# Kernel optimization log

Measured on AMD Instinct MI355X. Metric: run time of the kernel, lower is better.

## Reference

```python
import jax, jax.numpy as jnp
import numpy as np

N_NODES = 100000
N_EDGES = 1600000
N_GRAPHS = 64
D_IN = 128
D_HID = 128
PERM = 128
N_CLS = 8


def _sage_conv(h, src, dst, W_self, W_neigh, b, n_nodes):
    # DGL SAGEConv 'mean': fc_self(h) + fc_neigh(mean of in-neighbor feats) + bias
    agg = jax.ops.segment_sum(h[src], dst, num_segments=n_nodes)          # [N, d]
    deg = jax.ops.segment_sum(jnp.ones((src.shape[0],), h.dtype), dst,
                              num_segments=n_nodes)                        # [N]
    mean = agg / jnp.maximum(deg, 1.0)[:, None]                            # zero-deg nodes -> 0
    return h @ W_self + mean @ W_neigh + b


def setup_inputs() -> dict:
    key = jax.random.key(0)
    ks = jax.random.split(key, 12)
    s = 1.0 / np.sqrt(D_IN)
    inp = {
        'h': jax.random.normal(ks[0], (N_NODES, D_IN), jnp.float32),
        'perm_features': jax.random.normal(ks[1], (N_GRAPHS, PERM), jnp.float32),
        'src': jax.random.randint(ks[2], (N_EDGES,), 0, N_NODES),
        'dst': jax.random.randint(ks[3], (N_EDGES,), 0, N_NODES),
        'graph_ids': jnp.sort(jax.random.randint(ks[4], (N_NODES,), 0, N_GRAPHS)),
        'W1_self': jax.random.normal(ks[5], (D_IN, D_HID), jnp.float32) * s,
        'W1_neigh': jax.random.normal(ks[6], (D_IN, D_HID), jnp.float32) * s,
        'b1': jnp.zeros((D_HID,), jnp.float32),
        'W2_self': jax.random.normal(ks[7], (D_HID, D_HID), jnp.float32) * s,
        'W2_neigh': jax.random.normal(ks[8], (D_HID, D_HID), jnp.float32) * s,
        'b2': jnp.zeros((D_HID,), jnp.float32),
        'Wc': jax.random.normal(ks[9], (D_HID + PERM, N_CLS), jnp.float32) * s,
        'bc': jnp.zeros((N_CLS,), jnp.float32),
    }
    return inp


def reference(h, perm_features, src, dst, graph_ids,
              W1_self, W1_neigh, b1, W2_self, W2_neigh, b2, Wc, bc):
    n = h.shape[0]
    h1 = jax.nn.relu(_sage_conv(h, src, dst, W1_self, W1_neigh, b1, n))
    h2 = _sage_conv(h1, src, dst, W2_self, W2_neigh, b2, n)
    # dgl.mean_nodes: per-graph mean of node features
    gsum = jax.ops.segment_sum(h2, graph_ids, num_segments=N_GRAPHS)       # [B, d]
    gcnt = jax.ops.segment_sum(jnp.ones((n,), h.dtype), graph_ids,
                               num_segments=N_GRAPHS)                       # [B]
    hg = gsum / jnp.maximum(gcnt, 1.0)[:, None]
    combined = jnp.concatenate([hg, perm_features], axis=1)                 # [B, d+perm]
    return combined @ Wc + bc
```

## Files before the change

kernel.cpp:

```cpp
#include <hip/hip_runtime.h>

#define DID 128
#define NCLS 8
#define NPB 512
#define NPB_SHIFT 9
#define NBLK 256
#define CAP 12288
#define PCHUNK 64

typedef __attribute__((ext_vector_type(8))) short bf16x8;
typedef __attribute__((ext_vector_type(4))) float f32x4;
typedef __attribute__((ext_vector_type(8))) unsigned short u16x8;

static __device__ __forceinline__ unsigned short f2bf(float f) {
  union { float f; unsigned int u; } x;
  x.f = f;
  unsigned int r = (x.u + 0x7fffu + ((x.u >> 16) & 1u)) >> 16;
  return (unsigned short)r;
}
static __device__ __forceinline__ float bfhi(unsigned int v) {
  union { unsigned int u; float f; } x;
  x.u = v & 0xffff0000u;
  return x.f;
}
static __device__ __forceinline__ float bflo(unsigned int v) {
  union { unsigned int u; float f; } x;
  x.u = v << 16;
  return x.f;
}
static __device__ __forceinline__ int lowerb(const int* __restrict__ a, int n,
                                             int key) {
  int lo = 0, hi = n;
  while (lo < hi) {
    int m = (lo + hi) >> 1;
    if (a[m] < key) lo = m + 1;
    else hi = m;
  }
  return lo;
}

__global__ __launch_bounds__(256) void k_prep(
    const float* __restrict__ h, unsigned short* __restrict__ hb, int total8,
    int ncvt, const float* __restrict__ W0, const float* __restrict__ W1,
    const float* __restrict__ W2, const float* __restrict__ W3,
    unsigned short* __restrict__ P0, unsigned short* __restrict__ P1,
    unsigned short* __restrict__ P2, unsigned short* __restrict__ P3,
    const int* __restrict__ dst, int* __restrict__ hist, int E, int nbuk,
    float* __restrict__ gsum, int ngsum) {
  __shared__ int c[256];
  int bid = blockIdx.x;
  int tid = threadIdx.x;
  if (bid < ncvt) {
    int i = bid * 256 + tid;
    if (i >= total8) return;
    const float4* h4 = (const float4*)h;
    float4 a = h4[(size_t)i * 2];
    float4 b = h4[(size_t)i * 2 + 1];
    u16x8 o;
    o[0] = f2bf(a.x); o[1] = f2bf(a.y); o[2] = f2bf(a.z); o[3] = f2bf(a.w);
    o[4] = f2bf(b.x); o[5] = f2bf(b.y); o[6] = f2bf(b.z); o[7] = f2bf(b.w);
    *(u16x8*)(hb + (size_t)i * 8) = o;
  } else if (bid < ncvt + 256) {
    int gid = (bid - ncvt) * 256 + tid;
    int m = gid >> 14;
    int idx = gid & 16383;
    int j = idx & 7;
    int l = (idx >> 3) & 63;
    int kf = (idx >> 9) & 3;
    int ct = idx >> 11;
    int colc = ct * 16 + (l & 15);
    int k = kf * 32 + (l >> 4) * 8 + j;
    const float* W = (m == 0) ? W0 : (m == 1) ? W1 : (m == 2) ? W2 : W3;
    unsigned short* P = (m == 0) ? P0 : (m == 1) ? P1 : (m == 2) ? P2 : P3;
    P[idx] = f2bf(W[k * 128 + colc]);
  } else if (bid < ncvt + 256 + NBLK) {
    int b = bid - ncvt - 256;
    for (int i = tid; i < nbuk; i += 256) c[i] = 0;
    __syncthreads();
    int epb = (E + NBLK - 1) / NBLK;
    int e0 = b * epb;
    int e1 = min(E, e0 + epb);
    for (int e = e0 + tid; e < e1; e += 256)
      atomicAdd(&c[dst[e] >> NPB_SHIFT], 1);
    __syncthreads();
    for (int i = tid; i < nbuk; i += 256)
      hist[(size_t)i * NBLK + b] = c[i];
  } else {
    for (int i = tid; i < ngsum; i += 256) gsum[i] = 0.f;
  }
}

__global__ void k_scan1(const int* __restrict__ deg, int* __restrict__ rp,
                        int* __restrict__ part, int n) {
  __shared__ int sd[256];
  int t = threadIdx.x;
  int base = blockIdx.x * 1024 + t * 4;
  int v0 = (base + 0 < n) ? deg[base + 0] : 0;
  int v1 = (base + 1 < n) ? deg[base + 1] : 0;
  int v2 = (base + 2 < n) ? deg[base + 2] : 0;
  int v3 = (base + 3 < n) ? deg[base + 3] : 0;
  int ts = v0 + v1 + v2 + v3;
  sd[t] = ts;
  __syncthreads();
  for (int off = 1; off < 256; off <<= 1) {
    int x = 0;
    if (t >= off) x = sd[t - off];
    __syncthreads();
    if (t >= off) sd[t] += x;
    __syncthreads();
  }
  int excl = sd[t] - ts;
  if (base + 0 < n) rp[base + 0] = excl;
  if (base + 1 < n) rp[base + 1] = excl + v0;
  if (base + 2 < n) rp[base + 2] = excl + v0 + v1;
  if (base + 3 < n) rp[base + 3] = excl + v0 + v1 + v2;
  if (t == 255) part[blockIdx.x] = sd[255];
}

__global__ void k_scan2(int* __restrict__ part, int nblk) {
  __shared__ int sd[1024];
  int t = threadIdx.x;
  int v = (t < nblk) ? part[t] : 0;
  sd[t] = v;
  __syncthreads();
  for (int off = 1; off < 1024; off <<= 1) {
    int x = 0;
    if (t >= off) x = sd[t - off];
    __syncthreads();
    if (t >= off) sd[t] += x;
    __syncthreads();
  }
  if (t < nblk) part[t] = sd[t] - v;
}

__global__ void k_scan3(int* __restrict__ rp, const int* __restrict__ part,
                        int n, int E) {
  int t = threadIdx.x;
  int add = part[blockIdx.x];
  int base = blockIdx.x * 1024 + t * 4;
#pragma unroll
  for (int i = 0; i < 4; ++i)
    if (base + i < n) rp[base + i] += add;
  if (blockIdx.x == 0 && t == 0) rp[n] = E;
}

__global__ __launch_bounds__(256) void kB_scat(const int* __restrict__ src,
                                               const int* __restrict__ dst,
                                               const int* __restrict__ off,
                                               unsigned int* __restrict__ pairs,
                                               int E, int nbuk) {
  __shared__ int cur[256];
  int tid = threadIdx.x;
  for (int i = tid; i < nbuk; i += 256)
    cur[i] = off[(size_t)i * NBLK + blockIdx.x];
  __syncthreads();
  int epb = (E + NBLK - 1) / NBLK;
  int e0 = blockIdx.x * epb;
  int e1 = min(E, e0 + epb);
  for (int e = e0 + tid; e < e1; e += 256) {
    int s = src[e];
    int d = dst[e];
    int p = atomicAdd(&cur[d >> NPB_SHIFT], 1);
    pairs[p] = ((unsigned)(d & (NPB - 1)) << 23) | (unsigned)s;
  }
}

__global__ __launch_bounds__(512) void kB_build(
    const unsigned int* __restrict__ pairs, const int* __restrict__ off,
    int* __restrict__ rp, int* __restrict__ col, int N, int nbuk, int E) {
  __shared__ int cnt[NPB];
  __shared__ int exc[NPB];
  __shared__ int colstage[CAP];
  int tid = threadIdx.x;
  int b = blockIdx.x;
  int eb = off[(size_t)b * NBLK];
  int ee = off[(size_t)(b + 1) * NBLK];
  int m = ee - eb;

  cnt[tid] = 0;
  __syncthreads();
  for (int i = eb + tid; i < ee; i += NPB) {
    int dl = (int)(pairs[i] >> 23);
    atomicAdd(&cnt[dl], 1);
  }
  __syncthreads();
  exc[tid] = cnt[tid];
  __syncthreads();
  for (int o = 1; o < NPB; o <<= 1) {
    int v = (tid >= o) ? exc[tid - o] : 0;
    __syncthreads();
    exc[tid] += v;
    __syncthreads();
  }
  int myexc = exc[tid] - cnt[tid];
  int node = b * NPB + tid;
  if (node < N) rp[node] = eb + myexc;
  if (b == nbuk - 1 && tid == 0) rp[N] = E;
  __syncthreads();
  cnt[tid] = myexc;
  __syncthreads();
  if (m <= CAP) {
    for (int i = eb + tid; i < ee; i += NPB) {
      unsigned int pr = pairs[i];
      int dl = (int)(pr >> 23);
      int s = (int)(pr & 0x7fffffu);
      int p = atomicAdd(&cnt[dl], 1);
      colstage[p] = s;
    }
    __syncthreads();
    for (int i = tid; i < m; i += NPB) col[eb + i] = colstage[i];
  } else {
    for (int i = eb + tid; i < ee; i += NPB) {
      unsigned int pr = pairs[i];
      int dl = (int)(pr >> 23);
      int s = (int)(pr & 0x7fffffu);
      int p = atomicAdd(&cnt[dl], 1);
      col[eb + p] = s;
    }
  }
}

__global__ __launch_bounds__(256, 4) void k_gemm2(
    const unsigned short* __restrict__ hb, const unsigned short* __restrict__ WpS,
    const unsigned short* __restrict__ WpN, float* __restrict__ z,
    unsigned short* __restrict__ yb, int n) {
  const int l = threadIdx.x & 63;
  const int w = threadIdx.x >> 6;
  const int rb = blockIdx.x >> 1;
  const int cb = blockIdx.x & 1;
  const int rowW = rb * 128 + w * 32;
  const int cl = l & 15;
  const int cg = l >> 4;

  bf16x8 A[2][4];
#pragma unroll
  for (int rt = 0; rt < 2; ++rt) {
    int row = rowW + rt * 16 + cl;
#pragma unroll
    for (int kf = 0; kf < 4; ++kf) {
      if (row < n)
        A[rt][kf] = *(const bf16x8*)(hb + (size_t)row * 128 + kf * 32 + cg * 8);
      else
        A[rt][kf] = (bf16x8){0, 0, 0, 0, 0, 0, 0, 0};
    }
  }

  f32x4 accS[2][4], accN[2][4];
#pragma unroll
  for (int rt = 0; rt < 2; ++rt)
#pragma unroll
    for (int ct = 0; ct < 4; ++ct) {
      accS[rt][ct] = (f32x4){0.f, 0.f, 0.f, 0.f};
      accN[rt][ct] = (f32x4){0.f, 0.f, 0.f, 0.f};
    }

#pragma unroll
  for (int ct = 0; ct < 4; ++ct) {
    int ctg = cb * 4 + ct;
    bf16x8 BS[4], BN[4];
#pragma unroll
    for (int kf = 0; kf < 4; ++kf) {
      BS[kf] = *(const bf16x8*)(WpS + ((ctg * 4 + kf) * 64 + l) * 8);
      BN[kf] = *(const bf16x8*)(WpN + ((ctg * 4 + kf) * 64 + l) * 8);
    }
#pragma unroll
    for (int rt = 0; rt < 2; ++rt)
#pragma unroll
      for (int kf = 0; kf < 4; ++kf) {
        accS[rt][ct] =
            __builtin_amdgcn_mfma_f32_16x16x32_bf16(A[rt][kf], BS[kf], accS[rt][ct], 0, 0, 0);
        accN[rt][ct] =
            __builtin_amdgcn_mfma_f32_16x16x32_bf16(A[rt][kf], BN[kf], accN[rt][ct], 0, 0, 0);
      }
  }

#pragma unroll
  for (int rt = 0; rt < 2; ++rt)
#pragma unroll
    for (int ct = 0; ct < 4; ++ct) {
      int colc = (cb * 4 + ct) * 16 + cl;
#pragma unroll
      for (int r = 0; r < 4; ++r) {
        int row = rowW + rt * 16 + cg * 4 + r;
        if (row < n) {
          z[(size_t)row * 128 + colc] = accS[rt][ct][r];
          yb[(size_t)row * 128 + colc] = f2bf(accN[rt][ct][r]);
        }
      }
    }
}

template <int OUTMODE>
__global__ __launch_bounds__(256, 8) void k_aggr2(
    const unsigned int* __restrict__ Y, const float* Z,
    const int* __restrict__ rp, const int* __restrict__ col,
    const float* __restrict__ bias, void* outp, int n) {
  int wid = (blockIdx.x * 256 + threadIdx.x) >> 6;
  int lane = threadIdx.x & 63;
  if (wid >= n) return;
  int s = rp[wid], e = rp[wid + 1];
  float ax = 0.f, ay = 0.f;
  int i = s;
  for (; i + 8 <= e; i += 8) {
    unsigned int v0 = Y[(size_t)col[i + 0] * 64 + lane];
    unsigned int v1 = Y[(size_t)col[i + 1] * 64 + lane];
    unsigned int v2 = Y[(size_t)col[i + 2] * 64 + lane];
    unsigned int v3 = Y[(size_t)col[i + 3] * 64 + lane];
    unsigned int v4 = Y[(size_t)col[i + 4] * 64 + lane];
    unsigned int v5 = Y[(size_t)col[i + 5] * 64 + lane];
    unsigned int v6 = Y[(size_t)col[i + 6] * 64 + lane];
    unsigned int v7 = Y[(size_t)col[i + 7] * 64 + lane];
    ax += bflo(v0) + bflo(v1) + bflo(v2) + bflo(v3) + bflo(v4) + bflo(v5) +
          bflo(v6) + bflo(v7);
    ay += bfhi(v0) + bfhi(v1) + bfhi(v2) + bfhi(v3) + bfhi(v4) + bfhi(v5) +
          bfhi(v6) + bfhi(v7);
  }
  for (; i + 4 <= e; i += 4) {
    unsigned int v0 = Y[(size_t)col[i + 0] * 64 + lane];
    unsigned int v1 = Y[(size_t)col[i + 1] * 64 + lane];
    unsigned int v2 = Y[(size_t)col[i + 2] * 64 + lane];
    unsigned int v3 = Y[(size_t)col[i + 3] * 64 + lane];
    ax += bflo(v0) + bflo(v1) + bflo(v2) + bflo(v3);
    ay += bfhi(v0) + bfhi(v1) + bfhi(v2) + bfhi(v3);
  }
  for (; i < e; ++i) {
    unsigned int v = Y[(size_t)col[i] * 64 + lane];
    ax += bflo(v);
    ay += bfhi(v);
  }
  int deg = e - s;
  float scale = 1.0f / (float)(deg > 1 ? deg : 1);
  float2 zv = ((const float2*)Z)[(size_t)wid * 64 + lane];
  float2 bb = ((const float2*)bias)[lane];
  float ox = zv.x + ax * scale + bb.x;
  float oy = zv.y + ay * scale + bb.y;
  if (OUTMODE == 1) {
    ox = fmaxf(ox, 0.f);
    oy = fmaxf(oy, 0.f);
    unsigned int packed = (unsigned int)f2bf(ox) | ((unsigned int)f2bf(oy) << 16);
    ((unsigned int*)outp)[(size_t)wid * 64 + lane] = packed;
  } else {
    ((float2*)outp)[(size_t)wid * 64 + lane] = make_float2(ox, oy);
  }
}

__global__ __launch_bounds__(256) void k_pool(const float* __restrict__ H2,
                                              const int* __restrict__ gids,
                                              float* __restrict__ gsum, int N) {
  int g = blockIdx.x / PCHUNK;
  int c = blockIdx.x % PCHUNK;
  int t = threadIdx.x;
  int s = lowerb(gids, N, g);
  int e = lowerb(gids, N, g + 1);
  int cnt = e - s;
  int per = (cnt + PCHUNK - 1) / PCHUNK;
  int rs = s + c * per;
  int re = rs + per < e ? rs + per : e;
  if (rs >= re) return;
  int rslot = t >> 5;
  int d4 = t & 31;
  const float4* H4 = (const float4*)H2;
  float4 acc = make_float4(0.f, 0.f, 0.f, 0.f);
  for (int r = rs + rslot; r < re; r += 8) {
    float4 v = H4[(size_t)r * 32 + d4];
    acc.x += v.x; acc.y += v.y; acc.z += v.z; acc.w += v.w;
  }
  __shared__ float4 sacc[256];
  sacc[t] = acc;
  __syncthreads();
#pragma unroll
  for (int o = 4; o >= 1; o >>= 1) {
    if (rslot < o) {
      float4 a = sacc[t];
      float4 b = sacc[t + o * 32];
      a.x += b.x; a.y += b.y; a.z += b.z; a.w += b.w;
      sacc[t] = a;
    }
    __syncthreads();
  }
  if (t < 32) {
    float4 a = sacc[t];
    atomicAdd(&gsum[g * DID + t * 4 + 0], a.x);
    atomicAdd(&gsum[g * DID + t * 4 + 1], a.y);
    atomicAdd(&gsum[g * DID + t * 4 + 2], a.z);
    atomicAdd(&gsum[g * DID + t * 4 + 3], a.w);
  }
}

__global__ void k_head(const float* __restrict__ gsum,
                       const float* __restrict__ perm,
                       const float* __restrict__ Wc,
                       const float* __restrict__ bc,
                       const int* __restrict__ gids, float* __restrict__ out,
                       int N, int NG) {
  int t = threadIdx.x;
  if (t >= NG * NCLS) return;
  int g = t >> 3, c = t & 7;
  int cnt = lowerb(gids, N, g + 1) - lowerb(gids, N, g);
  float inv = 1.0f / (float)(cnt > 1 ? cnt : 1);
  float acc = bc[c];
#pragma unroll 4
  for (int k = 0; k < DID; ++k)
    acc += gsum[g * DID + k] * inv * Wc[k * NCLS + c];
#pragma unroll 4
  for (int k = 0; k < DID; ++k)
    acc += perm[g * DID + k] * Wc[(DID + k) * NCLS + c];
  out[g * NCLS + c] = acc;
}

extern "C" void kernel_launch(void* const* d_in, const int* in_sizes, int n_in,
                              void* d_out, int out_size, void* d_ws,
                              size_t ws_size, hipStream_t stream) {
  const float* h = (const float*)d_in[0];
  const float* perm = (const float*)d_in[1];
  const int* src = (const int*)d_in[2];
  const int* dst = (const int*)d_in[3];
  const int* gids = (const int*)d_in[4];
  const float* W1s = (const float*)d_in[5];
  const float* W1n = (const float*)d_in[6];
  const float* b1 = (const float*)d_in[7];
  const float* W2s = (const float*)d_in[8];
  const float* W2n = (const float*)d_in[9];
  const float* b2 = (const float*)d_in[10];
  const float* Wc = (const float*)d_in[11];
  const float* bc = (const float*)d_in[12];
  float* out = (float*)d_out;

  const int N = in_sizes[0] / DID;
  const int E = in_sizes[2];
  const int NG = in_sizes[1] / DID;
  const int nbuk = (N + NPB - 1) >> NPB_SHIFT;
  const int nscan = nbuk * NBLK;

  char* w = (char*)d_ws;
  size_t off_ = 0;
  auto alloc = [&](size_t bytes) -> void* {
    off_ = (off_ + 511) & ~(size_t)511;
    void* p = w + off_;
    off_ += bytes;
    return p;
  };
  float* gsum = (float*)alloc((size_t)NG * DID * 4);
  int* hist = (int*)alloc((size_t)nscan * 4);
  int* boff = (int*)alloc((size_t)(nscan + 1) * 4);
  int* part = (int*)alloc(1024 * 4);
  int* rp = (int*)alloc((size_t)(N + 1) * 4);
  int* col = (int*)alloc((size_t)E * 4);
  unsigned int* pairs = (unsigned int*)alloc((size_t)E * 4);
  unsigned short* hb = (unsigned short*)alloc((size_t)N * DID * 2);
  unsigned short* yb = (unsigned short*)alloc((size_t)N * DID * 2);
  float* z = (float*)alloc((size_t)N * DID * 4);
  unsigned short* Wp1s = (unsigned short*)alloc(128 * 128 * 2);
  unsigned short* Wp1n = (unsigned short*)alloc(128 * 128 * 2);
  unsigned short* Wp2s = (unsigned short*)alloc(128 * 128 * 2);
  unsigned short* Wp2n = (unsigned short*)alloc(128 * 128 * 2);

  const int nchunk = (nscan + 1023) / 1024;
  const int ngb2 = ((N + 127) / 128) * 2;
  const int nagg = (N + 3) / 4;
  const int total8 = N * DID / 8;
  const int ncvt = (total8 + 255) / 256;

  k_prep<<<ncvt + 256 + NBLK + 1, 256, 0, stream>>>(
      h, hb, total8, ncvt, W1s, W1n, W2s, W2n, Wp1s, Wp1n, Wp2s, Wp2n, dst,
      hist, E, nbuk, gsum, NG * DID);

  k_scan1<<<nchunk, 256, 0, stream>>>(hist, boff, part, nscan);
  k_scan2<<<1, 1024, 0, stream>>>(part, nchunk);
  k_scan3<<<nchunk, 256, 0, stream>>>(boff, part, nscan, E);
  kB_scat<<<NBLK, 256, 0, stream>>>(src, dst, boff, pairs, E, nbuk);
  kB_build<<<nbuk, NPB, 0, stream>>>(pairs, boff, rp, col, N, nbuk, E);

  k_gemm2<<<ngb2, 256, 0, stream>>>(hb, Wp1s, Wp1n, z, yb, N);
  k_aggr2<1><<<nagg, 256, 0, stream>>>((const unsigned int*)yb, z, rp, col, b1,
                                       (void*)hb, N);

  k_gemm2<<<ngb2, 256, 0, stream>>>(hb, Wp2s, Wp2n, z, yb, N);
  k_aggr2<0><<<nagg, 256, 0, stream>>>((const unsigned int*)yb, z, rp, col, b2,
                                       (void*)z, N);

  k_pool<<<NG * PCHUNK, 256, 0, stream>>>(z, gids, gsum, N);
  k_head<<<1, 512, 0, stream>>>(gsum, perm, Wc, bc, gids, out, N, NG);
}
```

Before: 421.0 us.

## Merge pipeline stages into fewer launches and fuse pool with head

Cuts the launch count by merging stages. The three-kernel scan becomes a single-block scan, and the bf16 conversion of h runs alongside it. The edge scatter and the first GEMM share one launch. The GEMM now computes all 128 columns per block rather than splitting columns across two blocks. Pooling and the classifier head are fused through a global atomic counter that block 0 spin-waits on, which assumes all blocks become resident and adds a serialized single-block scan.

```diff
diff --git a/kernel.cpp b/kernel.cpp
--- a/kernel.cpp
+++ b/kernel.cpp
@@ -6,7 +6,7 @@
 #define NPB_SHIFT 9
 #define NBLK 256
 #define CAP 12288
-#define PCHUNK 64
+#define PCHUNK 16
 
 typedef __attribute__((ext_vector_type(8))) short bf16x8;
 typedef __attribute__((ext_vector_type(4))) float f32x4;
@@ -39,29 +39,28 @@
   return lo;
 }
 
-__global__ __launch_bounds__(256) void k_prep(
-    const float* __restrict__ h, unsigned short* __restrict__ hb, int total8,
-    int ncvt, const float* __restrict__ W0, const float* __restrict__ W1,
+__global__ __launch_bounds__(256) void kA_hpz(
+    const int* __restrict__ dst, int* __restrict__ hist, int E, int nbuk,
+    const float* __restrict__ W0, const float* __restrict__ W1,
     const float* __restrict__ W2, const float* __restrict__ W3,
     unsigned short* __restrict__ P0, unsigned short* __restrict__ P1,
     unsigned short* __restrict__ P2, unsigned short* __restrict__ P3,
-    const int* __restrict__ dst, int* __restrict__ hist, int E, int nbuk,
     float* __restrict__ gsum, int ngsum) {
   __shared__ int c[256];
-  int bid = blockIdx.x;
-  int tid = threadIdx.x;
-  if (bid < ncvt) {
-    int i = bid * 256 + tid;
-    if (i >= total8) return;
-    const float4* h4 = (const float4*)h;
-    float4 a = h4[(size_t)i * 2];
-    float4 b = h4[(size_t)i * 2 + 1];
-    u16x8 o;
-    o[0] = f2bf(a.x); o[1] = f2bf(a.y); o[2] = f2bf(a.z); o[3] = f2bf(a.w);
-    o[4] = f2bf(b.x); o[5] = f2bf(b.y); o[6] = f2bf(b.z); o[7] = f2bf(b.w);
-    *(u16x8*)(hb + (size_t)i * 8) = o;
-  } else if (bid < ncvt + 256) {
-    int gid = (bid - ncvt) * 256 + tid;
+  int bid = blockIdx.x, tid = threadIdx.x;
+  if (bid < NBLK) {
+    for (int i = tid; i < nbuk; i += 256) c[i] = 0;
+    __syncthreads();
+    int epb = (E + NBLK - 1) / NBLK;
+    int e0 = bid * epb;
+    int e1 = min(E, e0 + epb);
+    for (int e = e0 + tid; e < e1; e += 256)
+      atomicAdd(&c[dst[e] >> NPB_SHIFT], 1);
+    __syncthreads();
+    for (int i = tid; i < nbuk; i += 256)
+      hist[(size_t)i * NBLK + bid] = c[i];
+  } else if (bid < NBLK + 256) {
+    int gid = (bid - NBLK) * 256 + tid;
     int m = gid >> 14;
     int idx = gid & 16383;
     int j = idx & 7;
@@ -73,96 +72,149 @@
     const float* W = (m == 0) ? W0 : (m == 1) ? W1 : (m == 2) ? W2 : W3;
     unsigned short* P = (m == 0) ? P0 : (m == 1) ? P1 : (m == 2) ? P2 : P3;
     P[idx] = f2bf(W[k * 128 + colc]);
-  } else if (bid < ncvt + 256 + NBLK) {
-    int b = bid - ncvt - 256;
-    for (int i = tid; i < nbuk; i += 256) c[i] = 0;
-    __syncthreads();
-    int epb = (E + NBLK - 1) / NBLK;
-    int e0 = b * epb;
-    int e1 = min(E, e0 + epb);
-    for (int e = e0 + tid; e < e1; e += 256)
-      atomicAdd(&c[dst[e] >> NPB_SHIFT], 1);
-    __syncthreads();
-    for (int i = tid; i < nbuk; i += 256)
-      hist[(size_t)i * NBLK + b] = c[i];
   } else {
     for (int i = tid; i < ngsum; i += 256) gsum[i] = 0.f;
   }
 }
 
-__global__ void k_scan1(const int* __restrict__ deg, int* __restrict__ rp,
-                        int* __restrict__ part, int n) {
-  __shared__ int sd[256];
-  int t = threadIdx.x;
-  int base = blockIdx.x * 1024 + t * 4;
-  int v0 = (base + 0 < n) ? deg[base + 0] : 0;
-  int v1 = (base + 1 < n) ? deg[base + 1] : 0;
-  int v2 = (base + 2 < n) ? deg[base + 2] : 0;
-  int v3 = (base + 3 < n) ? deg[base + 3] : 0;
-  int ts = v0 + v1 + v2 + v3;
-  sd[t] = ts;
-  __syncthreads();
-  for (int off = 1; off < 256; off <<= 1) {
-    int x = 0;
-    if (t >= off) x = sd[t - off];
-    __syncthreads();
-    if (t >= off) sd[t] += x;
-    __syncthreads();
-  }
-  int excl = sd[t] - ts;
-  if (base + 0 < n) rp[base + 0] = excl;
-  if (base + 1 < n) rp[base + 1] = excl + v0;
-  if (base + 2 < n) rp[base + 2] = excl + v0 + v1;
-  if (base + 3 < n) rp[base + 3] = excl + v0 + v1 + v2;
-  if (t == 255) part[blockIdx.x] = sd[255];
-}
-
-__global__ void k_scan2(int* __restrict__ part, int nblk) {
-  __shared__ int sd[1024];
-  int t = threadIdx.x;
-  int v = (t < nblk) ? part[t] : 0;
-  sd[t] = v;
-  __syncthreads();
-  for (int off = 1; off < 1024; off <<= 1) {
-    int x = 0;
-    if (t >= off) x = sd[t - off];
-    __syncthreads();
-    if (t >= off) sd[t] += x;
-    __syncthreads();
-  }
-  if (t < nblk) part[t] = sd[t] - v;
-}
-
-__global__ void k_scan3(int* __restrict__ rp, const int* __restrict__ part,
-                        int n, int E) {
-  int t = threadIdx.x;
-  int add = part[blockIdx.x];
-  int base = blockIdx.x * 1024 + t * 4;
-#pragma unroll
-  for (int i = 0; i < 4; ++i)
-    if (base + i < n) rp[base + i] += add;
-  if (blockIdx.x == 0 && t == 0) rp[n] = E;
-}
-
-__global__ __launch_bounds__(256) void kB_scat(const int* __restrict__ src,
-                                               const int* __restrict__ dst,
-                                               const int* __restrict__ off,
-                                               unsigned int* __restrict__ pairs,
-                                               int E, int nbuk) {
-  __shared__ int cur[256];
+__global__ __launch_bounds__(256) void kB_scan_h2b(
+    const int* __restrict__ hist, int* __restrict__ boff, int nbuk, int E,
+    const float* __restrict__ h, unsigned short* __restrict__ hb, int total8) {
   int tid = threadIdx.x;
-  for (int i = tid; i < nbuk; i += 256)
-    cur[i] = off[(size_t)i * NBLK + blockIdx.x];
-  __syncthreads();
-  int epb = (E + NBLK - 1) / NBLK;
-  int e0 = blockIdx.x * epb;
-  int e1 = min(E, e0 + epb);
-  for (int e = e0 + tid; e < e1; e += 256) {
-    int s = src[e];
-    int d = dst[e];
-    int p = atomicAdd(&cur[d >> NPB_SHIFT], 1);
-    pairs[p] = ((unsigned)(d & (NPB - 1)) << 23) | (unsigned)s;
-  }
+  if (blockIdx.x == 0) {
+    __shared__ int sd[256];
+    int seg = nbuk;
+    int base = tid * seg;
+    int ssum = 0;
+    for (int i = 0; i < seg; ++i) ssum += hist[base + i];
+    sd[tid] = ssum;
+    __syncthreads();
+    for (int o = 1; o < 256; o <<= 1) {
+      int x = (tid >= o) ? sd[tid - o] : 0;
+      __syncthreads();
+      sd[tid] += x;
+      __syncthreads();
+    }
+    int run = sd[tid] - ssum;
+    for (int i = 0; i < seg; ++i) {
+      int v = hist[base + i];
+      boff[base + i] = run;
+      run += v;
+    }
+    if (tid == 255) boff[(size_t)nbuk * NBLK] = E;
+  } else {
+    int i = (blockIdx.x - 1) * 256 + tid;
+    if (i >= total8) return;
+    const float4* h4 = (const float4*)h;
+    float4 a = h4[(size_t)i * 2];
+    float4 b = h4[(size_t)i * 2 + 1];
+    u16x8 o;
+    o[0] = f2bf(a.x); o[1] = f2bf(a.y); o[2] = f2bf(a.z); o[3] = f2bf(a.w);
+    o[4] = f2bf(b.x); o[5] = f2bf(b.y); o[6] = f2bf(b.z); o[7] = f2bf(b.w);
+    *(u16x8*)(hb + (size_t)i * 8) = o;
+  }
+}
+
+__device__ __forceinline__ void gemm_body(
+    int bid, const unsigned short* __restrict__ hb,
+    const unsigned short* __restrict__ WpS,
+    const unsigned short* __restrict__ WpN, float* __restrict__ z,
+    unsigned short* __restrict__ yb, int n) {
+  const int l = threadIdx.x & 63;
+  const int w = threadIdx.x >> 6;
+  const int rowW = bid * 128 + w * 32;
+  const int cl = l & 15;
+  const int cg = l >> 4;
+
+  bf16x8 A[2][4];
+#pragma unroll
+  for (int rt = 0; rt < 2; ++rt) {
+    int row = rowW + rt * 16 + cl;
+#pragma unroll
+    for (int kf = 0; kf < 4; ++kf) {
+      if (row < n)
+        A[rt][kf] = *(const bf16x8*)(hb + (size_t)row * 128 + kf * 32 + cg * 8);
+      else
+        A[rt][kf] = (bf16x8){0, 0, 0, 0, 0, 0, 0, 0};
+    }
+  }
+
+  f32x4 accS[2][8], accN[2][8];
+#pragma unroll
+  for (int rt = 0; rt < 2; ++rt)
+#pragma unroll
+    for (int ct = 0; ct < 8; ++ct) {
+      accS[rt][ct] = (f32x4){0.f, 0.f, 0.f, 0.f};
+      accN[rt][ct] = (f32x4){0.f, 0.f, 0.f, 0.f};
+    }
+
+#pragma unroll
+  for (int ct = 0; ct < 8; ++ct) {
+    bf16x8 BS[4], BN[4];
+#pragma unroll
+    for (int kf = 0; kf < 4; ++kf) {
+      BS[kf] = *(const bf16x8*)(WpS + ((ct * 4 + kf) * 64 + l) * 8);
+      BN[kf] = *(const bf16x8*)(WpN + ((ct * 4 + kf) * 64 + l) * 8);
+    }
+#pragma unroll
+    for (int rt = 0; rt < 2; ++rt)
+#pragma unroll
+      for (int kf = 0; kf < 4; ++kf) {
+        accS[rt][ct] =
+            __builtin_amdgcn_mfma_f32_16x16x32_bf16(A[rt][kf], BS[kf], accS[rt][ct], 0, 0, 0);
+        accN[rt][ct] =
+            __builtin_amdgcn_mfma_f32_16x16x32_bf16(A[rt][kf], BN[kf], accN[rt][ct], 0, 0, 0);
+      }
+  }
+
+#pragma unroll
+  for (int rt = 0; rt < 2; ++rt)
+#pragma unroll
+    for (int ct = 0; ct < 8; ++ct) {
+#pragma unroll
+      for (int r = 0; r < 4; ++r) {
+        int row = rowW + rt * 16 + cg * 4 + r;
+        if (row < n) {
+          int colc = ct * 16 + cl;
+          z[(size_t)row * 128 + colc] = accS[rt][ct][r];
+          yb[(size_t)row * 128 + colc] = f2bf(accN[rt][ct][r]);
+        }
+      }
+    }
+}
+
+__global__ __launch_bounds__(256) void kC_scat_gemm(
+    const int* __restrict__ src, const int* __restrict__ dst,
+    const int* __restrict__ boff, unsigned int* __restrict__ pairs, int E,
+    int nbuk, const unsigned short* __restrict__ hb,
+    const unsigned short* __restrict__ WpS,
+    const unsigned short* __restrict__ WpN, float* __restrict__ z,
+    unsigned short* __restrict__ yb, int n) {
+  int bid = blockIdx.x, tid = threadIdx.x;
+  if (bid < NBLK) {
+    __shared__ int cur[256];
+    for (int i = tid; i < nbuk; i += 256)
+      cur[i] = boff[(size_t)i * NBLK + bid];
+    __syncthreads();
+    int epb = (E + NBLK - 1) / NBLK;
+    int e0 = bid * epb;
+    int e1 = min(E, e0 + epb);
+    for (int e = e0 + tid; e < e1; e += 256) {
+      int s = src[e];
+      int d = dst[e];
+      int p = atomicAdd(&cur[d >> NPB_SHIFT], 1);
+      pairs[p] = ((unsigned)(d & (NPB - 1)) << 23) | (unsigned)s;
+    }
+  } else {
+    gemm_body(bid - NBLK, hb, WpS, WpN, z, yb, n);
+  }
+}
+
+__global__ __launch_bounds__(256, 2) void k_gemmS(
+    const unsigned short* __restrict__ hb, const unsigned short* __restrict__ WpS,
+    const unsigned short* __restrict__ WpN, float* __restrict__ z,
+    unsigned short* __restrict__ yb, int n) {
+  gemm_body(blockIdx.x, hb, WpS, WpN, z, yb, n);
 }
 
 __global__ __launch_bounds__(512) void kB_build(
@@ -218,76 +270,6 @@
       col[eb + p] = s;
     }
   }
-}
-
-__global__ __launch_bounds__(256, 4) void k_gemm2(
-    const unsigned short* __restrict__ hb, const unsigned short* __restrict__ WpS,
-    const unsigned short* __restrict__ WpN, float* __restrict__ z,
-    unsigned short* __restrict__ yb, int n) {
-  const int l = threadIdx.x & 63;
-  const int w = threadIdx.x >> 6;
-  const int rb = blockIdx.x >> 1;
-  const int cb = blockIdx.x & 1;
-  const int rowW = rb * 128 + w * 32;
-  const int cl = l & 15;
-  const int cg = l >> 4;
-
-  bf16x8 A[2][4];
-#pragma unroll
-  for (int rt = 0; rt < 2; ++rt) {
-    int row = rowW + rt * 16 + cl;
-#pragma unroll
-    for (int kf = 0; kf < 4; ++kf) {
-      if (row < n)
-        A[rt][kf] = *(const bf16x8*)(hb + (size_t)row * 128 + kf * 32 + cg * 8);
-      else
-        A[rt][kf] = (bf16x8){0, 0, 0, 0, 0, 0, 0, 0};
-    }
-  }
-
-  f32x4 accS[2][4], accN[2][4];
-#pragma unroll
-  for (int rt = 0; rt < 2; ++rt)
-#pragma unroll
-    for (int ct = 0; ct < 4; ++ct) {
-      accS[rt][ct] = (f32x4){0.f, 0.f, 0.f, 0.f};
-      accN[rt][ct] = (f32x4){0.f, 0.f, 0.f, 0.f};
-    }
-
-#pragma unroll
-  for (int ct = 0; ct < 4; ++ct) {
-    int ctg = cb * 4 + ct;
-    bf16x8 BS[4], BN[4];
-#pragma unroll
-    for (int kf = 0; kf < 4; ++kf) {
-      BS[kf] = *(const bf16x8*)(WpS + ((ctg * 4 + kf) * 64 + l) * 8);
-      BN[kf] = *(const bf16x8*)(WpN + ((ctg * 4 + kf) * 64 + l) * 8);
-    }
-#pragma unroll
-    for (int rt = 0; rt < 2; ++rt)
-#pragma unroll
-      for (int kf = 0; kf < 4; ++kf) {
-        accS[rt][ct] =
-            __builtin_amdgcn_mfma_f32_16x16x32_bf16(A[rt][kf], BS[kf], accS[rt][ct], 0, 0, 0);
-        accN[rt][ct] =
-            __builtin_amdgcn_mfma_f32_16x16x32_bf16(A[rt][kf], BN[kf], accN[rt][ct], 0, 0, 0);
-      }
-  }
-
-#pragma unroll
-  for (int rt = 0; rt < 2; ++rt)
-#pragma unroll
-    for (int ct = 0; ct < 4; ++ct) {
-      int colc = (cb * 4 + ct) * 16 + cl;
-#pragma unroll
-      for (int r = 0; r < 4; ++r) {
-        int row = rowW + rt * 16 + cg * 4 + r;
-        if (row < n) {
-          z[(size_t)row * 128 + colc] = accS[rt][ct][r];
-          yb[(size_t)row * 128 + colc] = f2bf(accN[rt][ct][r]);
-        }
-      }
-    }
 }
 
 template <int OUTMODE>
@@ -344,68 +326,80 @@
   }
 }
 
-__global__ __launch_bounds__(256) void k_pool(const float* __restrict__ H2,
-                                              const int* __restrict__ gids,
-                                              float* __restrict__ gsum, int N) {
-  int g = blockIdx.x / PCHUNK;
-  int c = blockIdx.x % PCHUNK;
-  int t = threadIdx.x;
+__global__ __launch_bounds__(256) void kF_pool_head(
+    const float* __restrict__ H2, const int* __restrict__ gids,
+    float* __restrict__ gsum, const float* __restrict__ perm,
+    const float* __restrict__ Wc, const float* __restrict__ bc,
+    float* __restrict__ out, int N, int NG, int* __restrict__ sync) {
+  int bid = blockIdx.x, t = threadIdx.x;
+  int g = bid / PCHUNK;
+  int c = bid % PCHUNK;
   int s = lowerb(gids, N, g);
   int e = lowerb(gids, N, g + 1);
   int cnt = e - s;
   int per = (cnt + PCHUNK - 1) / PCHUNK;
   int rs = s + c * per;
   int re = rs + per < e ? rs + per : e;
-  if (rs >= re) return;
-  int rslot = t >> 5;
-  int d4 = t & 31;
-  const float4* H4 = (const float4*)H2;
-  float4 acc = make_float4(0.f, 0.f, 0.f, 0.f);
-  for (int r = rs + rslot; r < re; r += 8) {
-    float4 v = H4[(size_t)r * 32 + d4];
-    acc.x += v.x; acc.y += v.y; acc.z += v.z; acc.w += v.w;
-  }
   __shared__ float4 sacc[256];
-  sacc[t] = acc;
-  __syncthreads();
-#pragma unroll
-  for (int o = 4; o >= 1; o >>= 1) {
-    if (rslot < o) {
+  if (rs < re) {
+    int rslot = t >> 5;
+    int d4 = t & 31;
+    const float4* H4 = (const float4*)H2;
+    float4 acc = make_float4(0.f, 0.f, 0.f, 0.f);
+    for (int r = rs + rslot; r < re; r += 8) {
+      float4 v = H4[(size_t)r * 32 + d4];
+      acc.x += v.x; acc.y += v.y; acc.z += v.z; acc.w += v.w;
+    }
+    sacc[t] = acc;
+    __syncthreads();
+#pragma unroll
+    for (int o = 4; o >= 1; o >>= 1) {
+      if (rslot < o) {
+        float4 a = sacc[t];
+        float4 b = sacc[t + o * 32];
+        a.x += b.x; a.y += b.y; a.z += b.z; a.w += b.w;
+        sacc[t] = a;
+      }
+      __syncthreads();
+    }
+    if (t < 32) {
       float4 a = sacc[t];
-      float4 b = sacc[t + o * 32];
-      a.x += b.x; a.y += b.y; a.z += b.z; a.w += b.w;
-      sacc[t] = a;
-    }
-    __syncthreads();
-  }
-  if (t < 32) {
-    float4 a = sacc[t];
-    atomicAdd(&gsum[g * DID + t * 4 + 0], a.x);
-    atomicAdd(&gsum[g * DID + t * 4 + 1], a.y);
-    atomicAdd(&gsum[g * DID + t * 4 + 2], a.z);
-    atomicAdd(&gsum[g * DID + t * 4 + 3], a.w);
-  }
-}
-
-__global__ void k_head(const float* __restrict__ gsum,
-                       const float* __restrict__ perm,
-                       const float* __restrict__ Wc,
-                       const float* __restrict__ bc,
-                       const int* __restrict__ gids, float* __restrict__ out,
-                       int N, int NG) {
-  int t = threadIdx.x;
-  if (t >= NG * NCLS) return;
-  int g = t >> 3, c = t & 7;
-  int cnt = lowerb(gids, N, g + 1) - lowerb(gids, N, g);
-  float inv = 1.0f / (float)(cnt > 1 ? cnt : 1);
-  float acc = bc[c];
+      atomicAdd(&gsum[g * DID + t * 4 + 0], a.x);
+      atomicAdd(&gsum[g * DID + t * 4 + 1], a.y);
+      atomicAdd(&gsum[g * DID + t * 4 + 2], a.z);
+      atomicAdd(&gsum[g * DID + t * 4 + 3], a.w);
+    }
+  }
+  __syncthreads();
+  if (t == 0) {
+    __threadfence();
+    __hip_atomic_fetch_add(&sync[3], 1, __ATOMIC_ACQ_REL,
+                           __HIP_MEMORY_SCOPE_AGENT);
+  }
+  if (bid != 0) return;
+  if (t == 0) {
+    while (__hip_atomic_load(&sync[3], __ATOMIC_ACQUIRE,
+                             __HIP_MEMORY_SCOPE_AGENT) < (int)gridDim.x) {
+      __builtin_amdgcn_s_sleep(4);
+    }
+    __threadfence();
+  }
+  __syncthreads();
+  for (int idx = t; idx < NG * NCLS; idx += 256) {
+    int gg = idx >> 3, cc = idx & 7;
+    int gcnt = lowerb(gids, N, gg + 1) - lowerb(gids, N, gg);
+    float inv = 1.0f / (float)(gcnt > 1 ? gcnt : 1);
+    float acc = bc[cc];
 #pragma unroll 4
-  for (int k = 0; k < DID; ++k)
-    acc += gsum[g * DID + k] * inv * Wc[k * NCLS + c];
+    for (int k = 0; k < DID; ++k)
+      acc += __hip_atomic_load(&gsum[gg * DID + k], __ATOMIC_RELAXED,
+                               __HIP_MEMORY_SCOPE_AGENT) *
+             inv * Wc[k * NCLS + cc];
 #pragma unroll 4
-  for (int k = 0; k < DID; ++k)
-    acc += perm[g * DID + k] * Wc[(DID + k) * NCLS + c];
-  out[g * NCLS + c] = acc;
+    for (int k = 0; k < DID; ++k)
+      acc += perm[gg * DID + k] * Wc[(DID + k) * NCLS + cc];
+    out[gg * NCLS + cc] = acc;
+  }
 }
 
 extern "C" void kernel_launch(void* const* d_in, const int* in_sizes, int n_in,
@@ -440,10 +434,10 @@
     off_ += bytes;
     return p;
   };
+  int* sync = (int*)alloc(8 * 4);
   float* gsum = (float*)alloc((size_t)NG * DID * 4);
   int* hist = (int*)alloc((size_t)nscan * 4);
   int* boff = (int*)alloc((size_t)(nscan + 1) * 4);
-  int* part = (int*)alloc(1024 * 4);
   int* rp = (int*)alloc((size_t)(N + 1) * 4);
   int* col = (int*)alloc((size_t)E * 4);
   unsigned int* pairs = (unsigned int*)alloc((size_t)E * 4);
@@ -455,30 +449,25 @@
   unsigned short* Wp2s = (unsigned short*)alloc(128 * 128 * 2);
   unsigned short* Wp2n = (unsigned short*)alloc(128 * 128 * 2);
 
-  const int nchunk = (nscan + 1023) / 1024;
-  const int ngb2 = ((N + 127) / 128) * 2;
+  const int ngb = (N + 127) / 128;
   const int nagg = (N + 3) / 4;
   const int total8 = N * DID / 8;
   const int ncvt = (total8 + 255) / 256;
 
-  k_prep<<<ncvt + 256 + NBLK + 1, 256, 0, stream>>>(
-      h, hb, total8, ncvt, W1s, W1n, W2s, W2n, Wp1s, Wp1n, Wp2s, Wp2n, dst,
-      hist, E, nbuk, gsum, NG * DID);
-
-  k_scan1<<<nchunk, 256, 0, stream>>>(hist, boff, part, nscan);
-  k_scan2<<<1, 1024, 0, stream>>>(part, nchunk);
-  k_scan3<<<nchunk, 256, 0, stream>>>(boff, part, nscan, E);
-  kB_scat<<<NBLK, 256, 0, stream>>>(src, dst, boff, pairs, E, nbuk);
+  hipMemsetAsync(sync, 0, 8 * 4, stream);
+
+  kA_hpz<<<NBLK + 256 + 1, 256, 0, stream>>>(dst, hist, E, nbuk, W1s, W1n, W2s,
+                                             W2n, Wp1s, Wp1n, Wp2s, Wp2n, gsum,
+                                             NG * DID);
+  kB_scan_h2b<<<1 + ncvt, 256, 0, stream>>>(hist, boff, nbuk, E, h, hb, total8);
+  kC_scat_gemm<<<NBLK + ngb, 256, 0, stream>>>(src, dst, boff, pairs, E, nbuk,
+                                               hb, Wp1s, Wp1n, z, yb, N);
   kB_build<<<nbuk, NPB, 0, stream>>>(pairs, boff, rp, col, N, nbuk, E);
-
-  k_gemm2<<<ngb2, 256, 0, stream>>>(hb, Wp1s, Wp1n, z, yb, N);
   k_aggr2<1><<<nagg, 256, 0, stream>>>((const unsigned int*)yb, z, rp, col, b1,
                                        (void*)hb, N);
-
-  k_gemm2<<<ngb2, 256, 0, stream>>>(hb, Wp2s, Wp2n, z, yb, N);
+  k_gemmS<<<ngb, 256, 0, stream>>>(hb, Wp2s, Wp2n, z, yb, N);
   k_aggr2<0><<<nagg, 256, 0, stream>>>((const unsigned int*)yb, z, rp, col, b2,
                                        (void*)z, N);
-
-  k_pool<<<NG * PCHUNK, 256, 0, stream>>>(z, gids, gsum, N);
-  k_head<<<1, 512, 0, stream>>>(gsum, perm, Wc, bc, gids, out, N, NG);
-}
+  kF_pool_head<<<NG * PCHUNK, 256, 0, stream>>>(z, gids, gsum, perm, Wc, bc,
+                                                out, N, NG, sync);
+}
```

New measurement: 527.9 us. 1.25x slower.
